# Kernel optimization log

Measured on AMD Instinct MI355X. Metric: run time of the kernel, lower is better.

## Reference

```python
import jax, jax.numpy as jnp
import numpy as np

GROUP_SIZE = 128
INTERMEDIATE = 18944


def _unpack_int4(packed):
    # packed: [rows, cols//8] int32, 8 nibbles per int32 along output dim
    shifts = jnp.arange(8, dtype=jnp.int32) * 4
    nib = (packed[:, :, None] >> shifts) & 15  # [rows, cols//8, 8]
    return nib.reshape(packed.shape[0], packed.shape[1] * 8)


def awq_gemm(x, qweight, qzeros, scales, group_size):
    # Dequantize: W[i,j] = (w4[i,j] - z4[i//g, j]) * scales[i//g, j]
    w = _unpack_int4(qweight).astype(jnp.float32)           # [in, out]
    z = _unpack_int4(qzeros).astype(jnp.float32)            # [in//g, out]
    s = scales.astype(jnp.float32)                          # [in//g, out]
    W = ((w - jnp.repeat(z, group_size, axis=0)) * jnp.repeat(s, group_size, axis=0))
    return (x @ W.astype(x.dtype))                          # [tokens, out]


def setup_inputs() -> dict:
    key = jax.random.key(0)
    ks = jax.random.split(key, 7)
    imax = 2147483647
    return {
        "x": (jax.random.normal(ks[0], (4096, 3584), dtype=jnp.float32) * 0.02).astype(jnp.float16),
        "qweight_gu": jax.random.randint(ks[1], (3584, 4736), 0, imax, dtype=jnp.int32),
        "qzeros_gu": jax.random.randint(ks[2], (28, 4736), 0, imax, dtype=jnp.int32),
        "scales_gu": (jax.random.uniform(ks[3], (28, 37888), dtype=jnp.float32) * 0.01 + 0.001).astype(jnp.float16),
        "qweight_down": jax.random.randint(ks[4], (18944, 448), 0, imax, dtype=jnp.int32),
        "qzeros_down": jax.random.randint(ks[5], (148, 448), 0, imax, dtype=jnp.int32),
        "scales_down": (jax.random.uniform(ks[6], (148, 3584), dtype=jnp.float32) * 0.01 + 0.001).astype(jnp.float16),
    }


def reference(x, qweight_gu, qzeros_gu, scales_gu, qweight_down, qzeros_down, scales_down):
    # Fused gate+up AWQ GEMM (matches forward path after fuse_gate_up())
    gate_up = awq_gemm(x, qweight_gu, qzeros_gu, scales_gu, GROUP_SIZE)  # [T, 2*I]
    gate = gate_up[..., :INTERMEDIATE]
    up = gate_up[..., INTERMEDIATE:]
    intermediate = jax.nn.silu(gate) * up                                # fused SiLU*mul
    down = awq_gemm(intermediate, qweight_down, qzeros_down, scales_down, GROUP_SIZE)
    return down
```

## Files before the change

kernel.cpp:

```cpp
#include <hip/hip_runtime.h>
#include <hip/hip_fp16.h>
#include <stdint.h>

typedef _Float16 half8 __attribute__((ext_vector_type(8)));
typedef float f32x4 __attribute__((ext_vector_type(4)));

#define GLD_LDS16(gp, lp)                                                     \
  __builtin_amdgcn_global_load_lds(                                           \
      (const __attribute__((address_space(1))) void*)(gp),                    \
      (__attribute__((address_space(3))) void*)(lp), 16, 0, 0)

__global__ void xcvt_kernel(const float* __restrict__ in, __half* __restrict__ out) {
  const size_t i = ((size_t)blockIdx.x * 256 + threadIdx.x) * 4;
  float4 v = *(const float4*)(in + i);
  __half2* o = (__half2*)(out + i);
  o[0] = __floats2half2_rn(v.x, v.y);
  o[1] = __floats2half2_rn(v.z, v.w);
}

__global__ void repack_kernel(const int* __restrict__ qw, uint32_t* __restrict__ rp, int P) {
  const int N = P * 8;
  const int n = blockIdx.x * 256 + threadIdx.x;
  const int j8 = n >> 3;
  const int sh = (n & 7) * 4;
  #pragma unroll
  for (int qi = 0; qi < 4; ++qi) {
    const int q = blockIdx.y * 4 + qi;
    const int* src = qw + (size_t)(q * 8) * P + j8;
    uint32_t r = 0;
    #pragma unroll
    for (int t = 0; t < 8; ++t) {
      uint32_t w = ((uint32_t)src[t * P] >> sh) & 15u;
      r |= w << (4 * (t >> 1) + 16 * (t & 1));
    }
    rp[(size_t)q * N + n] = r;
  }
}

__global__ void smz_kernel(const float* __restrict__ sc, const int* __restrict__ qz,
                           uint32_t* __restrict__ smz, int P) {
  const int N = P * 8;
  const int n = blockIdx.x * 256 + threadIdx.x;
  const int g = blockIdx.y;
  uint32_t sbits = __half_as_ushort(__float2half(sc[(size_t)g * N + n]));
  uint32_t z = ((uint32_t)qz[(size_t)g * P + (n >> 3)] >> ((n & 7) * 4)) & 15u;
  uint32_t hz = 0x6400u | z;
  smz[(size_t)g * N + n] = sbits | (hz << 16);
}

union U32H2 { uint32_t u; __half2 h; };
__device__ inline uint32_t dq_pair(uint32_t t, uint32_t s2, uint32_t z2) {
  U32H2 a, s, z, r;
  a.u = t; s.u = s2; z.u = z2;
  r.h = __hmul2(__hsub2(a.h, z.h), s.h);
  return r.u;
}
__device__ inline half8 dequant8(uint32_t p, uint32_t s2, uint32_t z2) {
  union { uint32_t u[4]; half8 v; } r;
  r.u[0] = dq_pair((p & 0x000F000Fu) | 0x64006400u, s2, z2);
  r.u[1] = dq_pair(((p >> 4) & 0x000F000Fu) | 0x64006400u, s2, z2);
  r.u[2] = dq_pair(((p >> 8) & 0x000F000Fu) | 0x64006400u, s2, z2);
  r.u[3] = dq_pair(((p >> 12) & 0x000F000Fu) | 0x64006400u, s2, z2);
  return r.v;
}

template <int KDIM, int NW, int T1OFF, int OW, bool SILU, int NT, int BXS>
__global__ __launch_bounds__(256, 2) void awq_gemm(const __half* __restrict__ A,
                                                   const uint32_t* __restrict__ RP,
                                                   const uint32_t* __restrict__ SMZ,
                                                   void* __restrict__ OUT) {
  __shared__ __align__(16) unsigned char sA[2][128 * 64 * 2];
  __shared__ __align__(16) unsigned char sB[2][NT * 8 * 128 * 4];

  const int tid = threadIdx.x;
  const int l = tid & 63;
  const int wv = tid >> 6;
  const int l15 = l & 15;
  const int l4 = l >> 4;

  const int row0 = blockIdx.y * 128;
  const int n0 = blockIdx.x * BXS;

  const __half* asrc[4];
  #pragma unroll
  for (int it = 0; it < 4; ++it) {
    int m = it * 32 + (tid >> 3);
    int cs = tid & 7;
    int kc = cs ^ (m & 7);
    asrc[it] = A + (size_t)(row0 + m) * KDIM + kc * 8;
  }

  const uint32_t* bsrc[NT];
  #pragma unroll
  for (int it = 0; it < NT; ++it) {
    int idx = it * 256 + tid;
    int tile = idx >> 8;
    int qr = (idx >> 5) & 7;
    int l32 = idx & 31;
    int S = ((qr & 1) << 4) | ((qr >> 1) << 2);
    bsrc[it] = RP + (size_t)qr * NW + n0 + tile * T1OFF + ((l32 * 4) ^ S);
  }

  int colb[NT][2];
  #pragma unroll
  for (int tile = 0; tile < NT; ++tile)
    #pragma unroll
    for (int nf = 0; nf < 2; ++nf)
      colb[tile][nf] = n0 + wv * 32 + nf * 16 + l15 + (tile ? T1OFF : 0);

  f32x4 acc[NT][2][8];
  const f32x4 zero4 = {0.f, 0.f, 0.f, 0.f};
  #pragma unroll
  for (int t = 0; t < NT; ++t)
    #pragma unroll
    for (int nf = 0; nf < 2; ++nf)
      #pragma unroll
      for (int mf = 0; mf < 8; ++mf) acc[t][nf][mf] = zero4;

  uint32_t s2[NT][2], z2[NT][2], su[NT][2];

  constexpr int NSTEP = KDIM / 64;
  constexpr int NGRP = KDIM / 128;

  #pragma unroll
  for (int it = 0; it < 4; ++it)
    GLD_LDS16(asrc[it], &sA[0][it * 4096 + tid * 16]);
  #pragma unroll
  for (int it = 0; it < NT; ++it)
    GLD_LDS16(bsrc[it], &sB[0][(it * 256 + tid) * 16]);
  #pragma unroll
  for (int tile = 0; tile < NT; ++tile)
    #pragma unroll
    for (int nf = 0; nf < 2; ++nf)
      su[tile][nf] = SMZ[colb[tile][nf]];

  for (int t = 0; t < NSTEP; ++t) {
    const int cur = t & 1;
    __syncthreads();

    if (t + 1 < NSTEP) {
      #pragma unroll
      for (int it = 0; it < 4; ++it)
        GLD_LDS16(asrc[it] + (t + 1) * 64, &sA[cur ^ 1][it * 4096 + tid * 16]);
      #pragma unroll
      for (int it = 0; it < NT; ++it)
        GLD_LDS16(bsrc[it] + (size_t)(t + 1) * 8 * NW, &sB[cur ^ 1][(it * 256 + tid) * 16]);
    }

    if ((t & 1) == 0) {
      #pragma unroll
      for (int tile = 0; tile < NT; ++tile)
        #pragma unroll
        for (int nf = 0; nf < 2; ++nf) {
          uint32_t u = su[tile][nf];
          uint32_t lo = u & 0xFFFFu;
          s2[tile][nf] = lo | (lo << 16);
          z2[tile][nf] = (u & 0xFFFF0000u) | (u >> 16);
        }
      const int g1 = (t >> 1) + 1;
      if (g1 < NGRP) {
        #pragma unroll
        for (int tile = 0; tile < NT; ++tile)
          #pragma unroll
          for (int nf = 0; nf < 2; ++nf)
            su[tile][nf] = SMZ[(size_t)g1 * NW + colb[tile][nf]];
      }
    }

    uint32_t bq[2][NT][2];
    const int bro = wv * 32 + l15;
    #pragma unroll
    for (int kk = 0; kk < 2; ++kk) {
      const int Sl = ((l4 & 1) << 4) | (kk << 3) | ((l4 >> 1) << 2);
      #pragma unroll
      for (int tile = 0; tile < NT; ++tile)
        #pragma unroll
        for (int nf = 0; nf < 2; ++nf)
          bq[kk][tile][nf] = *(const uint32_t*)&sB[cur][
              (((tile * 8 + kk * 4 + l4) * 128) + ((bro + nf * 16) ^ Sl)) * 4];
    }

    const unsigned char* base = sA[cur];
    #pragma unroll
    for (int kk = 0; kk < 2; ++kk) {
      half8 a[8];
      #pragma unroll
      for (int mf = 0; mf < 8; ++mf) {
        int m = mf * 16 + l15;
        int chunk = (kk * 4 + l4) ^ (l15 & 7);
        a[mf] = *(const half8*)(base + m * 128 + chunk * 16);
      }
      #pragma unroll
      for (int tile = 0; tile < NT; ++tile)
        #pragma unroll
        for (int nf = 0; nf < 2; ++nf) {
          half8 b = dequant8(bq[kk][tile][nf], s2[tile][nf], z2[tile][nf]);
          #pragma unroll
          for (int mf = 0; mf < 8; ++mf)
            acc[tile][nf][mf] =
                __builtin_amdgcn_mfma_f32_16x16x32_f16(a[mf], b, acc[tile][nf][mf], 0, 0, 0);
        }
    }
  }

  if (SILU) {
    __half* O = (__half*)OUT;
    #pragma unroll
    for (int nf = 0; nf < 2; ++nf)
      #pragma unroll
      for (int mf = 0; mf < 8; ++mf)
        #pragma unroll
        for (int r = 0; r < 4; ++r) {
          int row = row0 + mf * 16 + l4 * 4 + r;
          int col = n0 + wv * 32 + nf * 16 + l15;
          float gf = __half2float(__float2half(acc[0][nf][mf][r]));
          float uf = __half2float(__float2half(acc[1][nf][mf][r]));
          float sig = 1.f / (1.f + __expf(-gf));
          float sil = __half2float(__float2half(gf * sig));
          O[(size_t)row * OW + col] = __float2half(sil * uf);
        }
  } else {
    float* O = (float*)OUT;
    #pragma unroll
    for (int tile = 0; tile < NT; ++tile)
      #pragma unroll
      for (int nf = 0; nf < 2; ++nf)
        #pragma unroll
        for (int mf = 0; mf < 8; ++mf)
          #pragma unroll
          for (int r = 0; r < 4; ++r) {
            int row = row0 + mf * 16 + l4 * 4 + r;
            int col = n0 + tile * T1OFF + wv * 32 + nf * 16 + l15;
            O[(size_t)row * OW + col] = __half2float(__float2half(acc[tile][nf][mf][r]));
          }
  }
}

extern "C" void kernel_launch(void* const* d_in, const int* in_sizes, int n_in,
                              void* d_out, int out_size, void* d_ws, size_t ws_size,
                              hipStream_t stream) {
  const float* x_f32 = (const float*)d_in[0];
  const int* qw_gu = (const int*)d_in[1];
  const int* qz_gu = (const int*)d_in[2];
  const float* sc_gu = (const float*)d_in[3];
  const int* qw_dn = (const int*)d_in[4];
  const int* qz_dn = (const int*)d_in[5];
  const float* sc_dn = (const float*)d_in[6];

  char* ws = (char*)d_ws;
  __half* interm   = (__half*)ws;
  uint32_t* rp_gu  = (uint32_t*)(ws + 155189248ull);
  uint32_t* smz_gu = (uint32_t*)(ws + 223084544ull);
  __half* xh       = (__half*)(ws + 227328000ull);
  uint32_t* rp_dn  = (uint32_t*)(ws + 155189248ull);
  uint32_t* smz_dn = (uint32_t*)(ws + 189136896ull);

  xcvt_kernel<<<14336, 256, 0, stream>>>(x_f32, xh);
  repack_kernel<<<dim3(148, 112), 256, 0, stream>>>(qw_gu, rp_gu, 4736);
  smz_kernel<<<dim3(148, 28), 256, 0, stream>>>(sc_gu, qz_gu, smz_gu, 4736);

  awq_gemm<3584, 37888, 18944, 18944, true, 2, 128>
      <<<dim3(148, 32), 256, 0, stream>>>(xh, rp_gu, smz_gu, (void*)interm);

  repack_kernel<<<dim3(14, 592), 256, 0, stream>>>(qw_dn, rp_dn, 448);
  smz_kernel<<<dim3(14, 148), 256, 0, stream>>>(sc_dn, qz_dn, smz_dn, 448);

  awq_gemm<18944, 3584, 128, 3584, false, 2, 256>
      <<<dim3(14, 32), 256, 0, stream>>>(interm, rp_dn, smz_dn, d_out);
}
```

Baseline: 1.692 ms.

## Triple-buffer LDS pipeline with explicit vmcnt waits and LDS-staged scale/zero loads

Replaces the double-buffered A/B shared-memory tiles with a three-stage ring that prefetches two K-steps ahead. Each step now waits on a partial vmcnt and a raw s_barrier instead of a full __syncthreads drain. Scale/zero words are fetched straight into LDS with 4-byte global_load_lds, replacing per-thread global register loads. Dequant is rewritten with native half2 vector ops. The hand-tuned vmcnt counts depend on how many loads are issued per step, and the larger LDS footprint may cut occupancy below the two blocks per CU set in launch bounds.

Measured after the change: 1.624 ms. 4.0% less time.

```diff
diff --git a/kernel.cpp b/kernel.cpp
--- a/kernel.cpp
+++ b/kernel.cpp
@@ -3,12 +3,17 @@
 #include <stdint.h>
 
 typedef _Float16 half8 __attribute__((ext_vector_type(8)));
+typedef _Float16 h2v __attribute__((ext_vector_type(2)));
 typedef float f32x4 __attribute__((ext_vector_type(4)));
 
 #define GLD_LDS16(gp, lp)                                                     \
   __builtin_amdgcn_global_load_lds(                                           \
       (const __attribute__((address_space(1))) void*)(gp),                    \
       (__attribute__((address_space(3))) void*)(lp), 16, 0, 0)
+#define GLD_LDS4(gp, lp)                                                      \
+  __builtin_amdgcn_global_load_lds(                                           \
+      (const __attribute__((address_space(1))) void*)(gp),                    \
+      (__attribute__((address_space(3))) void*)(lp), 4, 0, 0)
 
 __global__ void xcvt_kernel(const float* __restrict__ in, __half* __restrict__ out) {
   const size_t i = ((size_t)blockIdx.x * 256 + threadIdx.x) * 4;
@@ -48,20 +53,20 @@
   smz[(size_t)g * N + n] = sbits | (hz << 16);
 }
 
-union U32H2 { uint32_t u; __half2 h; };
-__device__ inline uint32_t dq_pair(uint32_t t, uint32_t s2, uint32_t z2) {
-  U32H2 a, s, z, r;
-  a.u = t; s.u = s2; z.u = z2;
-  r.h = __hmul2(__hsub2(a.h, z.h), s.h);
-  return r.u;
-}
-__device__ inline half8 dequant8(uint32_t p, uint32_t s2, uint32_t z2) {
-  union { uint32_t u[4]; half8 v; } r;
-  r.u[0] = dq_pair((p & 0x000F000Fu) | 0x64006400u, s2, z2);
-  r.u[1] = dq_pair(((p >> 4) & 0x000F000Fu) | 0x64006400u, s2, z2);
-  r.u[2] = dq_pair(((p >> 8) & 0x000F000Fu) | 0x64006400u, s2, z2);
-  r.u[3] = dq_pair(((p >> 12) & 0x000F000Fu) | 0x64006400u, s2, z2);
-  return r.v;
+union U32H2 { uint32_t u; h2v h; };
+__device__ inline h2v bith2(uint32_t u) { U32H2 t; t.u = u; return t.h; }
+__device__ inline half8 dequant8(uint32_t p, h2v s, h2v z) {
+  U32H2 t0, t1, t2, t3;
+  t0.u = (p & 0x000F000Fu) | 0x64006400u;
+  t1.u = ((p >> 4) & 0x000F000Fu) | 0x64006400u;
+  t2.u = ((p >> 8) & 0x000F000Fu) | 0x64006400u;
+  t3.u = ((p >> 12) & 0x000F000Fu) | 0x64006400u;
+  h2v v0 = (t0.h - z) * s;
+  h2v v1 = (t1.h - z) * s;
+  h2v v2 = (t2.h - z) * s;
+  h2v v3 = (t3.h - z) * s;
+  half8 r = {v0.x, v0.y, v1.x, v1.y, v2.x, v2.y, v3.x, v3.y};
+  return r;
 }
 
 template <int KDIM, int NW, int T1OFF, int OW, bool SILU, int NT, int BXS>
@@ -69,8 +74,11 @@
                                                    const uint32_t* __restrict__ RP,
                                                    const uint32_t* __restrict__ SMZ,
                                                    void* __restrict__ OUT) {
-  __shared__ __align__(16) unsigned char sA[2][128 * 64 * 2];
-  __shared__ __align__(16) unsigned char sB[2][NT * 8 * 128 * 4];
+  constexpr int ABUF = 128 * 64 * 2;
+  constexpr int BBUF = NT * 8 * 128 * 4;
+  constexpr int BOFF = 3 * ABUF;
+  constexpr int ZOFF = BOFF + 3 * BBUF;
+  __shared__ __align__(16) unsigned char smem[ZOFF + 2048];
 
   const int tid = threadIdx.x;
   const int l = tid & 63;
@@ -101,12 +109,7 @@
     bsrc[it] = RP + (size_t)qr * NW + n0 + tile * T1OFF + ((l32 * 4) ^ S);
   }
 
-  int colb[NT][2];
-  #pragma unroll
-  for (int tile = 0; tile < NT; ++tile)
-    #pragma unroll
-    for (int nf = 0; nf < 2; ++nf)
-      colb[tile][nf] = n0 + wv * 32 + nf * 16 + l15 + (tile ? T1OFF : 0);
+  const uint32_t* zsrc = SMZ + n0 + (size_t)(tid >> 7) * T1OFF + (tid & 127);
 
   f32x4 acc[NT][2][8];
   const f32x4 zero4 = {0.f, 0.f, 0.f, 0.f};
@@ -117,58 +120,60 @@
       #pragma unroll
       for (int mf = 0; mf < 8; ++mf) acc[t][nf][mf] = zero4;
 
-  uint32_t s2[NT][2], z2[NT][2], su[NT][2];
-
+  uint32_t s2[NT][2], z2[NT][2];
   constexpr int NSTEP = KDIM / 64;
-  constexpr int NGRP = KDIM / 128;
 
   #pragma unroll
   for (int it = 0; it < 4; ++it)
-    GLD_LDS16(asrc[it], &sA[0][it * 4096 + tid * 16]);
+    GLD_LDS16(asrc[it], &smem[it * 4096 + tid * 16]);
   #pragma unroll
   for (int it = 0; it < NT; ++it)
-    GLD_LDS16(bsrc[it], &sB[0][(it * 256 + tid) * 16]);
-  #pragma unroll
-  for (int tile = 0; tile < NT; ++tile)
-    #pragma unroll
-    for (int nf = 0; nf < 2; ++nf)
-      su[tile][nf] = SMZ[colb[tile][nf]];
-
+    GLD_LDS16(bsrc[it], &smem[BOFF + (it * 256 + tid) * 16]);
+  GLD_LDS4(zsrc, &smem[ZOFF + tid * 4]);
+  #pragma unroll
+  for (int it = 0; it < 4; ++it)
+    GLD_LDS16(asrc[it] + 64, &smem[ABUF + it * 4096 + tid * 16]);
+  #pragma unroll
+  for (int it = 0; it < NT; ++it)
+    GLD_LDS16(bsrc[it] + (size_t)8 * NW, &smem[BOFF + BBUF + (it * 256 + tid) * 16]);
+
+  int cur = 0, stg = 2;
   for (int t = 0; t < NSTEP; ++t) {
-    const int cur = t & 1;
-    __syncthreads();
-
-    if (t + 1 < NSTEP) {
+    if (t == NSTEP - 1)      asm volatile("s_waitcnt vmcnt(0)" ::: "memory");
+    else if (t & 1)          asm volatile("s_waitcnt vmcnt(7)" ::: "memory");
+    else                     asm volatile("s_waitcnt vmcnt(6)" ::: "memory");
+    __builtin_amdgcn_s_barrier();
+
+    if (t + 2 < NSTEP) {
       #pragma unroll
       for (int it = 0; it < 4; ++it)
-        GLD_LDS16(asrc[it] + (t + 1) * 64, &sA[cur ^ 1][it * 4096 + tid * 16]);
+        GLD_LDS16(asrc[it] + (size_t)(t + 2) * 64, &smem[stg * ABUF + it * 4096 + tid * 16]);
       #pragma unroll
       for (int it = 0; it < NT; ++it)
-        GLD_LDS16(bsrc[it] + (size_t)(t + 1) * 8 * NW, &sB[cur ^ 1][(it * 256 + tid) * 16]);
+        GLD_LDS16(bsrc[it] + (size_t)(t + 2) * 8 * NW,
+                  &smem[BOFF + stg * BBUF + (it * 256 + tid) * 16]);
+      if (((t + 2) & 1) == 0) {
+        const int g = (t + 2) >> 1;
+        GLD_LDS4(zsrc + (size_t)g * NW, &smem[ZOFF + (g & 1) * 1024 + tid * 4]);
+      }
     }
 
     if ((t & 1) == 0) {
+      const uint32_t* zl = (const uint32_t*)&smem[ZOFF + ((t >> 1) & 1) * 1024];
       #pragma unroll
       for (int tile = 0; tile < NT; ++tile)
         #pragma unroll
         for (int nf = 0; nf < 2; ++nf) {
-          uint32_t u = su[tile][nf];
+          uint32_t u = zl[tile * 128 + wv * 32 + nf * 16 + l15];
           uint32_t lo = u & 0xFFFFu;
           s2[tile][nf] = lo | (lo << 16);
           z2[tile][nf] = (u & 0xFFFF0000u) | (u >> 16);
         }
-      const int g1 = (t >> 1) + 1;
-      if (g1 < NGRP) {
-        #pragma unroll
-        for (int tile = 0; tile < NT; ++tile)
-          #pragma unroll
-          for (int nf = 0; nf < 2; ++nf)
-            su[tile][nf] = SMZ[(size_t)g1 * NW + colb[tile][nf]];
-      }
     }
 
     uint32_t bq[2][NT][2];
     const int bro = wv * 32 + l15;
+    const unsigned char* bbase = &smem[BOFF + cur * BBUF];
     #pragma unroll
     for (int kk = 0; kk < 2; ++kk) {
       const int Sl = ((l4 & 1) << 4) | (kk << 3) | ((l4 >> 1) << 2);
@@ -176,11 +181,11 @@
       for (int tile = 0; tile < NT; ++tile)
         #pragma unroll
         for (int nf = 0; nf < 2; ++nf)
-          bq[kk][tile][nf] = *(const uint32_t*)&sB[cur][
+          bq[kk][tile][nf] = *(const uint32_t*)&bbase[
               (((tile * 8 + kk * 4 + l4) * 128) + ((bro + nf * 16) ^ Sl)) * 4];
     }
 
-    const unsigned char* base = sA[cur];
+    const unsigned char* abase = &smem[cur * ABUF];
     #pragma unroll
     for (int kk = 0; kk < 2; ++kk) {
       half8 a[8];
@@ -188,19 +193,22 @@
       for (int mf = 0; mf < 8; ++mf) {
         int m = mf * 16 + l15;
         int chunk = (kk * 4 + l4) ^ (l15 & 7);
-        a[mf] = *(const half8*)(base + m * 128 + chunk * 16);
+        a[mf] = *(const half8*)(abase + m * 128 + chunk * 16);
       }
       #pragma unroll
       for (int tile = 0; tile < NT; ++tile)
         #pragma unroll
         for (int nf = 0; nf < 2; ++nf) {
-          half8 b = dequant8(bq[kk][tile][nf], s2[tile][nf], z2[tile][nf]);
+          half8 b = dequant8(bq[kk][tile][nf], bith2(s2[tile][nf]), bith2(z2[tile][nf]));
           #pragma unroll
           for (int mf = 0; mf < 8; ++mf)
             acc[tile][nf][mf] =
                 __builtin_amdgcn_mfma_f32_16x16x32_f16(a[mf], b, acc[tile][nf][mf], 0, 0, 0);
         }
     }
+
+    cur = (cur == 2) ? 0 : cur + 1;
+    stg = (stg == 2) ? 0 : stg + 1;
   }
 
   if (SILU) {
```
